# Kernel optimization log

Measured on AMD Instinct MI355X. Metric: run time of the kernel, lower is better.

## Reference

```python
import jax, jax.numpy as jnp
import numpy as np

B, N, D, K, DSPACE, NFREQ = 4, 4096, 256, 16, 3, 5
BN_EPS = 1e-5


def setup_inputs() -> dict:
    key = jax.random.key(0)
    ks = jax.random.split(key, 12)
    s = 1.0 / np.sqrt(D)
    pe_in = DSPACE * 2 * NFREQ + DSPACE  # 33
    return {
        "xyz": jax.random.normal(ks[0], (B, N, DSPACE), jnp.float32),
        "feats": jax.random.normal(ks[1], (B, N, D), jnp.float32),
        "w_q": jax.random.uniform(ks[2], (D, D), jnp.float32, -s, s),
        "w_k": jax.random.uniform(ks[3], (D, D), jnp.float32, -s, s),
        "w_v": jax.random.uniform(ks[4], (D, D), jnp.float32, -s, s),
        "g_w1": jax.random.uniform(ks[5], (D, D), jnp.float32, -s, s),
        "g_b1": jax.random.uniform(ks[6], (D,), jnp.float32, -s, s),
        "g_w2": jax.random.uniform(ks[7], (D, D), jnp.float32, -s, s),
        "g_b2": jax.random.uniform(ks[8], (D,), jnp.float32, -s, s),
        "pe_w": jax.random.uniform(ks[9], (D, pe_in), jnp.float32, -s, s),
        "pe_b": jax.random.uniform(ks[10], (D,), jnp.float32, -s, s),
        "bn_w": jnp.ones((D,), jnp.float32),
        "bn_b": jnp.zeros((D,), jnp.float32),
    }


def _gather_knn(points, idx):
    # points [b,n,c], idx [b,n,k] -> [b,n,k,c]
    return jax.vmap(lambda p, i: p[i])(points, idx)


def reference(xyz, feats, w_q, w_k, w_v, g_w1, g_b1, g_w2, g_b2, pe_w, pe_b, bn_w, bn_b):
    # KNN (no grad in original): full pairwise sq-distance + top-k smallest
    dists = jnp.sum((xyz[:, :, None] - xyz[:, None]) ** 2, axis=-1)  # [b,n,n]
    _, knn_idx = jax.lax.top_k(-dists, K)  # [b,n,k], ascending distance
    knn_idx = jax.lax.stop_gradient(knn_idx)
    knn_xyz = jax.lax.stop_gradient(_gather_knn(xyz, knn_idx))  # [b,n,k,3]

    q = feats @ w_q.T                               # [b,n,d]
    k_g = _gather_knn(feats @ w_k.T, knn_idx)       # [b,n,k,d]
    v_g = _gather_knn(feats @ w_v.T, knn_idx)       # [b,n,k,d]

    pos_diff = xyz[:, :, None] - knn_xyz            # [b,n,k,3]
    freqs = jnp.linspace(1.0, 2.0 ** NFREQ, NFREQ).astype(pos_diff.dtype)
    embeds = [pos_diff]
    for f in freqs:
        embeds.append(jnp.sin(pos_diff * f))
        embeds.append(jnp.cos(pos_diff * f))
    pos_embed = jnp.concatenate(embeds, axis=-1)    # [b,n,k,33]
    pos_encode = pos_embed @ pe_w.T + pe_b          # [b,n,k,d]

    edges = q[:, :, None] - k_g + pos_encode        # [b,n,k,d]
    h = jax.nn.relu(edges @ g_w1.T + g_b1)
    attn = h @ g_w2.T + g_b2                        # [b,n,k,d]
    attn = jax.nn.softmax(attn, axis=-2)            # softmax over neighbors

    res = jnp.einsum('bnkf,bnkf->bnf', attn, v_g + pos_encode) + feats

    # BatchNorm1d over channel dim, training-mode batch stats (biased var)
    mean = jnp.mean(res, axis=(0, 1))
    var = jnp.var(res, axis=(0, 1))
    res = (res - mean) * jax.lax.rsqrt(var + BN_EPS) * bn_w + bn_b
    return res
```

## Files before the change

kernel.cpp:

```cpp
#include <hip/hip_runtime.h>

#define BB 4
#define NN 4096
#define DD 256
#define KK 16
#define PTS 2
#define SA 280
#define SE 104

typedef __bf16 bf16;
typedef __attribute__((ext_vector_type(8))) __bf16 bf16x8;
typedef __attribute__((ext_vector_type(4))) __bf16 bf16x4;
typedef __attribute__((ext_vector_type(4))) float f32x4;

__global__ __launch_bounds__(256, 2) void setup_kernel(
    const float* __restrict__ xyz, const float* __restrict__ feats,
    const float* __restrict__ w_q, const float* __restrict__ w_k,
    const float* __restrict__ w_v, const float* __restrict__ g_w1,
    const float* __restrict__ g_w2, const float* __restrict__ pe_w,
    int* __restrict__ knn, bf16* __restrict__ qb, bf16* __restrict__ kfb,
    bf16* __restrict__ vfb, bf16* __restrict__ w1b, bf16* __restrict__ w2b,
    bf16* __restrict__ pwb, float* __restrict__ sums) {
  const int bid = blockIdx.x;
  const int t = threadIdx.x;
  __shared__ __align__(16) bf16 fs[16][SA];

  if (bid < 256) {
    const int idx = bid * 256 + t;
    w1b[idx] = (bf16)g_w1[idx];
    w2b[idx] = (bf16)g_w2[idx];
    if (idx < 256 * 64) {
      const int n = idx >> 6, c = idx & 63;
      pwb[idx] = (c < 33) ? (bf16)pe_w[n * 33 + c] : (bf16)0.f;
    }
    if (idx < 2 * DD) sums[idx] = 0.f;
    return;
  }
  if (bid < 256 + 4096) {
    const int lane = t & 63;
    const int row = (bid - 256) * 4 + (t >> 6);
    const int b = row >> 12, i = row & (NN - 1);
    const float* xb = xyz + (size_t)b * NN * 3;
    const float xi = xb[i * 3 + 0], yi = xb[i * 3 + 1], zi = xb[i * 3 + 2];
    unsigned long long cand[64];
#pragma unroll
    for (int c = 0; c < 64; ++c) {
      const int j = c * 64 + lane;
      const float dx = xi - xb[j * 3 + 0];
      const float dy = yi - xb[j * 3 + 1];
      const float dz = zi - xb[j * 3 + 2];
      const float d = dx * dx + dy * dy + dz * dz;
      const unsigned long long fb =
          (unsigned long long)(__float_as_uint(d)) + 1ull;
      cand[c] = (fb << 32) | (unsigned int)j;
    }
    unsigned long long gm[8];
#pragma unroll
    for (int g = 0; g < 8; ++g) {
      unsigned long long mn = cand[g * 8];
#pragma unroll
      for (int s = 1; s < 8; ++s)
        if (cand[g * 8 + s] < mn) mn = cand[g * 8 + s];
      gm[g] = mn;
    }
    unsigned int myj = 0u;
    for (int r = 0; r < KK; ++r) {
      unsigned long long lmin = gm[0];
#pragma unroll
      for (int g = 1; g < 8; ++g)
        if (gm[g] < lmin) lmin = gm[g];
#pragma unroll
      for (int off = 1; off < 64; off <<= 1) {
        const unsigned long long o = __shfl_xor(lmin, off);
        if (o < lmin) lmin = o;
      }
      if (lane == r) myj = (unsigned int)lmin;
#pragma unroll
      for (int g = 0; g < 8; ++g) {
        if (__ballot(gm[g] == lmin)) {
          unsigned long long nm = ~0ull;
#pragma unroll
          for (int s = 0; s < 8; ++s) {
            const unsigned long long v = cand[g * 8 + s];
            if (v > lmin && v < nm) nm = v;
          }
          if (gm[g] == lmin) gm[g] = nm;
        }
      }
    }
    if (lane < KK) knn[row * KK + lane] = (int)myj;
    return;
  }
  {
    const int lane = t & 63, wv = t >> 6;
    const int m = lane & 15, qd = lane >> 4;
    const size_t r0 = (size_t)(bid - (256 + 4096)) * 16;
    const float4* f4 = (const float4*)(feats + r0 * DD);
#pragma unroll
    for (int i = 0; i < 4; ++i) {
      const int e = i * 256 + t;
      const float4 v = f4[e];
      bf16x4 w;
      w[0] = (bf16)v.x; w[1] = (bf16)v.y; w[2] = (bf16)v.z; w[3] = (bf16)v.w;
      *(bf16x4*)&fs[e >> 6][(e & 63) * 4] = w;
    }
    __syncthreads();
    bf16x8 afrag[8];
#pragma unroll
    for (int f = 0; f < 8; ++f)
      afrag[f] = *(const bf16x8*)&fs[m][f * 32 + qd * 8];
    const float* wmat[3] = {w_q, w_k, w_v};
    bf16* omat[3] = {qb, kfb, vfb};
    for (int mat = 0; mat < 3; ++mat) {
      const float* wb = wmat[mat];
      for (int nt = 0; nt < 4; ++nt) {
        const int n = wv * 64 + nt * 16 + m;
        bf16x8 bfr[8];
#pragma unroll
        for (int f = 0; f < 8; ++f) {
          const float4 wa = *(const float4*)(wb + (size_t)n * DD + f * 32 + qd * 8);
          const float4 wc = *(const float4*)(wb + (size_t)n * DD + f * 32 + qd * 8 + 4);
          bf16x8 x;
          x[0] = (bf16)wa.x; x[1] = (bf16)wa.y; x[2] = (bf16)wa.z; x[3] = (bf16)wa.w;
          x[4] = (bf16)wc.x; x[5] = (bf16)wc.y; x[6] = (bf16)wc.z; x[7] = (bf16)wc.w;
          bfr[f] = x;
        }
        f32x4 c = {0.f, 0.f, 0.f, 0.f};
#pragma unroll
        for (int f = 0; f < 8; ++f)
          c = __builtin_amdgcn_mfma_f32_16x16x32_bf16(afrag[f], bfr[f], c, 0, 0, 0);
#pragma unroll
        for (int rr = 0; rr < 4; ++rr)
          omat[mat][(r0 + qd * 4 + rr) * DD + n] = (bf16)c[rr];
      }
    }
  }
}

__global__ __launch_bounds__(256, 3) void edge_v7(
    const float* __restrict__ xyz, const float* __restrict__ feats,
    const bf16* __restrict__ qb, const bf16* __restrict__ kfb,
    const bf16* __restrict__ vfb, const int* __restrict__ knn,
    const bf16* __restrict__ w1b, const float* __restrict__ g_b1,
    const bf16* __restrict__ w2b, const float* __restrict__ g_b2,
    const bf16* __restrict__ pwb, const float* __restrict__ pe_b,
    float* __restrict__ res, float* __restrict__ sums,
    float* __restrict__ sumsq) {
  const int t = threadIdx.x;
  const int lane = t & 63;
  const int wv = t >> 6;
  const int m = lane & 15;
  const int qd = lane >> 4;
  const int row0 = blockIdx.x * PTS;
  const int b = row0 >> 12;

  __shared__ __align__(16) bf16 bufA[PTS][16][SA];
  __shared__ __align__(16) char un_s[PTS * 16 * SA * 2];
  bf16(*bufB)[16][SA] = (bf16(*)[16][SA])un_s;
  bf16(*emb_s)[16][SE] = (bf16(*)[16][SE])un_s;
  __shared__ int js_s[PTS][16];

  if (t < PTS * 16) js_s[t >> 4][t & 15] = knn[(row0 + (t >> 4)) * KK + (t & 15)];
  __syncthreads();

  const float* xb = xyz + (size_t)b * NN * 3;
  {
    const int k = t >> 4;
    const int c0 = (t & 15) * 6;
#pragma unroll
    for (int p = 0; p < PTS; ++p) {
      const int i = (row0 + p) & (NN - 1);
      const int j = js_s[p][k];
#pragma unroll
      for (int cc = 0; cc < 6; ++cc) {
        const int c = c0 + cc;
        float val = 0.f;
        if (c < 33) {
          const int ax = (c < 3) ? c : (c - 3) % 3;
          const float pd = xb[i * 3 + ax] - xb[j * 3 + ax];
          if (c < 3) {
            val = pd;
          } else {
            const int f = (c - 3) / 6;
            const float x = pd * fmaf(7.75f, (float)f, 1.0f);
            val = (((c - 3) % 6) < 3) ? __sinf(x) : __cosf(x);
          }
        }
        emb_s[p][k][c] = (bf16)val;
      }
    }
  }
  __syncthreads();

  float vpe[4][PTS][4];
  bf16x8 ea0[PTS], ea1[PTS];
#pragma unroll
  for (int p = 0; p < PTS; ++p) {
    ea0[p] = *(const bf16x8*)&emb_s[p][m][qd * 8];
    ea1[p] = *(const bf16x8*)&emb_s[p][m][32 + qd * 8];
  }
#pragma unroll
  for (int tt = 0; tt < 4; ++tt) {
    const int n = wv * 64 + tt * 16 + m;
    const bf16x8 b0 = *(const bf16x8*)(pwb + (size_t)n * 64 + qd * 8);
    const bf16x8 b1 = *(const bf16x8*)(pwb + (size_t)n * 64 + 32 + qd * 8);
    const float bias = pe_b[n];
#pragma unroll
    for (int p = 0; p < PTS; ++p) {
      f32x4 c = {bias, bias, bias, bias};
      c = __builtin_amdgcn_mfma_f32_16x16x32_bf16(ea0[p], b0, c, 0, 0, 0);
      c = __builtin_amdgcn_mfma_f32_16x16x32_bf16(ea1[p], b1, c, 0, 0, 0);
      const float qv = (float)qb[(size_t)(row0 + p) * DD + n];
#pragma unroll
      for (int rr = 0; rr < 4; ++rr) {
        const int krow = qd * 4 + rr;
        const size_t jr = ((size_t)(b * NN + js_s[p][krow])) * DD + n;
        bufA[p][krow][n] = (bf16)(qv - (float)kfb[jr] + c[rr]);
        vpe[tt][p][rr] = (float)vfb[jr] + c[rr];
      }
    }
  }
  __syncthreads();

  {
    bf16x8 afrag[PTS][8];
#pragma unroll
    for (int p = 0; p < PTS; ++p)
#pragma unroll
      for (int f = 0; f < 8; ++f)
        afrag[p][f] = *(const bf16x8*)&bufA[p][m][f * 32 + qd * 8];
    for (int tt = 0; tt < 4; ++tt) {
      const int n = wv * 64 + tt * 16 + m;
      bf16x8 bfr[8];
#pragma unroll
      for (int f = 0; f < 8; ++f)
        bfr[f] = *(const bf16x8*)(w1b + (size_t)n * DD + f * 32 + qd * 8);
      const float bias = g_b1[n];
#pragma unroll
      for (int p = 0; p < PTS; ++p) {
        f32x4 c = {bias, bias, bias, bias};
#pragma unroll
        for (int f = 0; f < 8; ++f)
          c = __builtin_amdgcn_mfma_f32_16x16x32_bf16(afrag[p][f], bfr[f], c, 0, 0, 0);
#pragma unroll
        for (int rr = 0; rr < 4; ++rr)
          bufB[p][qd * 4 + rr][n] = (bf16)fmaxf(c[rr], 0.f);
      }
    }
  }
  __syncthreads();

  {
    bf16x8 afrag[PTS][8];
#pragma unroll
    for (int p = 0; p < PTS; ++p)
#pragma unroll
      for (int f = 0; f < 8; ++f)
        afrag[p][f] = *(const bf16x8*)&bufB[p][m][f * 32 + qd * 8];
#pragma unroll
    for (int tt = 0; tt < 4; ++tt) {
      const int n = wv * 64 + tt * 16 + m;
      bf16x8 bfr[8];
#pragma unroll
      for (int f = 0; f < 8; ++f)
        bfr[f] = *(const bf16x8*)(w2b + (size_t)n * DD + f * 32 + qd * 8);
      const float bias = g_b2[n];
      float bs = 0.f, bs2 = 0.f;
#pragma unroll
      for (int p = 0; p < PTS; ++p) {
        f32x4 c = {bias, bias, bias, bias};
#pragma unroll
        for (int f = 0; f < 8; ++f)
          c = __builtin_amdgcn_mfma_f32_16x16x32_bf16(afrag[p][f], bfr[f], c, 0, 0, 0);
        float mx = fmaxf(fmaxf(c[0], c[1]), fmaxf(c[2], c[3]));
        mx = fmaxf(mx, __shfl_xor(mx, 16));
        mx = fmaxf(mx, __shfl_xor(mx, 32));
        float e[4], den = 0.f;
#pragma unroll
        for (int rr = 0; rr < 4; ++rr) {
          e[rr] = __expf(c[rr] - mx);
          den += e[rr];
        }
        den += __shfl_xor(den, 16);
        den += __shfl_xor(den, 32);
        float num = 0.f;
#pragma unroll
        for (int rr = 0; rr < 4; ++rr) num += e[rr] * vpe[tt][p][rr];
        num += __shfl_xor(num, 16);
        num += __shfl_xor(num, 32);
        if (qd == 0) {
          const size_t o = (size_t)(row0 + p) * DD + n;
          const float out = num / den + feats[o];
          res[o] = out;
          bs += out;
          bs2 += out * out;
        }
      }
      if (qd == 0) {
        atomicAdd(&sums[n], bs);
        atomicAdd(&sumsq[n], bs2);
      }
    }
  }
}

__global__ __launch_bounds__(256) void bn_apply(float* __restrict__ out,
                                                const float* __restrict__ sums,
                                                const float* __restrict__ sumsq,
                                                const float* __restrict__ bn_w,
                                                const float* __restrict__ bn_b) {
  const int idx = blockIdx.x * 256 + threadIdx.x;
  const int c = idx & (DD - 1);
  const float inv_n = 1.f / (float)(BB * NN);
  const float mean = sums[c] * inv_n;
  const float var = sumsq[c] * inv_n - mean * mean;
  const float v = out[idx];
  out[idx] = (v - mean) * rsqrtf(var + 1e-5f) * bn_w[c] + bn_b[c];
}

extern "C" void kernel_launch(void* const* d_in, const int* in_sizes, int n_in,
                              void* d_out, int out_size, void* d_ws,
                              size_t ws_size, hipStream_t stream) {
  (void)in_sizes; (void)n_in; (void)out_size; (void)ws_size;
  const float* xyz = (const float*)d_in[0];
  const float* feats = (const float*)d_in[1];
  const float* w_q = (const float*)d_in[2];
  const float* w_k = (const float*)d_in[3];
  const float* w_v = (const float*)d_in[4];
  const float* g_w1 = (const float*)d_in[5];
  const float* g_b1 = (const float*)d_in[6];
  const float* g_w2 = (const float*)d_in[7];
  const float* g_b2 = (const float*)d_in[8];
  const float* pe_w = (const float*)d_in[9];
  const float* pe_b = (const float*)d_in[10];
  const float* bn_w = (const float*)d_in[11];
  const float* bn_b = (const float*)d_in[12];
  float* out = (float*)d_out;

  const int BN = BB * NN;
  char* w = (char*)d_ws;
  int* knn = (int*)w;       w += (size_t)BN * KK * 4;
  bf16* qb = (bf16*)w;      w += (size_t)BN * DD * 2;
  bf16* kfb = (bf16*)w;     w += (size_t)BN * DD * 2;
  bf16* vfb = (bf16*)w;     w += (size_t)BN * DD * 2;
  float* sums = (float*)w;  w += DD * 4;
  float* sumsq = (float*)w; w += DD * 4;
  bf16* w1b = (bf16*)w;     w += (size_t)DD * DD * 2;
  bf16* w2b = (bf16*)w;     w += (size_t)DD * DD * 2;
  bf16* pwb = (bf16*)w;     w += (size_t)DD * 64 * 2;

  setup_kernel<<<256 + 4096 + 1024, 256, 0, stream>>>(
      xyz, feats, w_q, w_k, w_v, g_w1, g_w2, pe_w, knn, qb, kfb, vfb, w1b, w2b,
      pwb, sums);
  edge_v7<<<BN / PTS, 256, 0, stream>>>(xyz, feats, qb, kfb, vfb, knn, w1b,
                                        g_b1, w2b, g_b2, pwb, pe_b, out, sums,
                                        sumsq);
  bn_apply<<<BN, 256, 0, stream>>>(out, sums, sumsq, bn_w, bn_b);
}
```

Baseline: 648.5 us.

## Stage xyz in LDS for KNN, enlarge projection tiles, use 512-thread edge blocks

In the setup kernel, the KNN branch now copies the whole batch's xyz into shared memory before the distance loop, replacing strided global reads. The projection branch handles 64 rows per block instead of 16, so each converted weight fragment is reused across four waves, and the block roles are reordered. The edge kernel moves to 512 threads per block, with each wave covering 32 output columns instead of 64, to cut per-thread register use and raise parallelism. The costs are a 48KB shared-memory staging copy per KNN block (limiting occupancy) and heavier LDS pressure per block in the edge kernel.

After: 907.2 us. 1.4x slower.

```diff
diff --git a/kernel.cpp b/kernel.cpp
--- a/kernel.cpp
+++ b/kernel.cpp
@@ -6,12 +6,16 @@
 #define KK 16
 #define PTS 2
 #define SA 280
-#define SE 104
+#define SE 96
 
 typedef __bf16 bf16;
 typedef __attribute__((ext_vector_type(8))) __bf16 bf16x8;
 typedef __attribute__((ext_vector_type(4))) __bf16 bf16x4;
 typedef __attribute__((ext_vector_type(4))) float f32x4;
+
+#define KNNB 4096
+#define PROJB 256
+#define PREPB 256
 
 __global__ __launch_bounds__(256, 2) void setup_kernel(
     const float* __restrict__ xyz, const float* __restrict__ feats,
@@ -23,10 +27,117 @@
     bf16* __restrict__ pwb, float* __restrict__ sums) {
   const int bid = blockIdx.x;
   const int t = threadIdx.x;
-  __shared__ __align__(16) bf16 fs[16][SA];
-
-  if (bid < 256) {
-    const int idx = bid * 256 + t;
+  __shared__ __align__(16) float smem[NN * 3];
+
+  if (bid < KNNB) {
+    const int row0 = bid * 4;
+    const int b = row0 >> 12;
+    const float* xb = xyz + (size_t)b * NN * 3;
+    for (int e = t; e < NN * 3; e += 256) smem[e] = xb[e];
+    __syncthreads();
+    const int lane = t & 63;
+    const int row = row0 + (t >> 6);
+    const int i = row & (NN - 1);
+    const float xi = smem[i * 3 + 0], yi = smem[i * 3 + 1], zi = smem[i * 3 + 2];
+    unsigned long long cand[64];
+#pragma unroll
+    for (int c = 0; c < 64; ++c) {
+      const int j = c * 64 + lane;
+      const float dx = xi - smem[j * 3 + 0];
+      const float dy = yi - smem[j * 3 + 1];
+      const float dz = zi - smem[j * 3 + 2];
+      const float d = dx * dx + dy * dy + dz * dz;
+      const unsigned long long fb =
+          (unsigned long long)(__float_as_uint(d)) + 1ull;
+      cand[c] = (fb << 32) | (unsigned int)j;
+    }
+    unsigned long long gm[8];
+#pragma unroll
+    for (int g = 0; g < 8; ++g) {
+      unsigned long long mn = cand[g * 8];
+#pragma unroll
+      for (int s = 1; s < 8; ++s)
+        if (cand[g * 8 + s] < mn) mn = cand[g * 8 + s];
+      gm[g] = mn;
+    }
+    unsigned int myj = 0u;
+    for (int r = 0; r < KK; ++r) {
+      unsigned long long lmin = gm[0];
+#pragma unroll
+      for (int g = 1; g < 8; ++g)
+        if (gm[g] < lmin) lmin = gm[g];
+#pragma unroll
+      for (int off = 1; off < 64; off <<= 1) {
+        const unsigned long long o = __shfl_xor(lmin, off);
+        if (o < lmin) lmin = o;
+      }
+      if (lane == r) myj = (unsigned int)lmin;
+#pragma unroll
+      for (int g = 0; g < 8; ++g) {
+        if (__ballot(gm[g] == lmin)) {
+          unsigned long long nm = ~0ull;
+#pragma unroll
+          for (int s = 0; s < 8; ++s) {
+            const unsigned long long v = cand[g * 8 + s];
+            if (v > lmin && v < nm) nm = v;
+          }
+          if (gm[g] == lmin) gm[g] = nm;
+        }
+      }
+    }
+    if (lane < KK) knn[row * KK + lane] = (int)myj;
+    return;
+  }
+  if (bid < KNNB + PROJB) {
+    bf16(*fs)[264] = (bf16(*)[264])smem;
+    const int lane = t & 63, wv = t >> 6;
+    const int m = lane & 15, qd = lane >> 4;
+    const size_t r0 = (size_t)(bid - KNNB) * 64;
+    const float4* f4 = (const float4*)(feats + r0 * DD);
+#pragma unroll
+    for (int i = 0; i < 16; ++i) {
+      const int e = i * 256 + t;
+      const float4 v = f4[e];
+      bf16x4 w;
+      w[0] = (bf16)v.x; w[1] = (bf16)v.y; w[2] = (bf16)v.z; w[3] = (bf16)v.w;
+      *(bf16x4*)&fs[e >> 6][(e & 63) * 4] = w;
+    }
+    __syncthreads();
+    bf16x8 afrag[8];
+#pragma unroll
+    for (int f = 0; f < 8; ++f)
+      afrag[f] = *(const bf16x8*)&fs[wv * 16 + m][f * 32 + qd * 8];
+    const float* wmat[3] = {w_q, w_k, w_v};
+    bf16* omat[3] = {qb, kfb, vfb};
+    for (int mat = 0; mat < 3; ++mat) {
+      const float* wb = wmat[mat];
+      for (int nt = 0; nt < 16; ++nt) {
+        const int n = nt * 16 + m;
+        bf16x8 bfr[8];
+#pragma unroll
+        for (int f = 0; f < 8; ++f) {
+          const float4 wa =
+              *(const float4*)(wb + (size_t)n * DD + f * 32 + qd * 8);
+          const float4 wc =
+              *(const float4*)(wb + (size_t)n * DD + f * 32 + qd * 8 + 4);
+          bf16x8 x;
+          x[0] = (bf16)wa.x; x[1] = (bf16)wa.y; x[2] = (bf16)wa.z; x[3] = (bf16)wa.w;
+          x[4] = (bf16)wc.x; x[5] = (bf16)wc.y; x[6] = (bf16)wc.z; x[7] = (bf16)wc.w;
+          bfr[f] = x;
+        }
+        f32x4 c = {0.f, 0.f, 0.f, 0.f};
+#pragma unroll
+        for (int f = 0; f < 8; ++f)
+          c = __builtin_amdgcn_mfma_f32_16x16x32_bf16(afrag[f], bfr[f], c, 0, 0, 0);
+#pragma unroll
+        for (int rr = 0; rr < 4; ++rr)
+          omat[mat][(r0 + wv * 16 + qd * 4 + rr) * DD + n] = (bf16)c[rr];
+      }
+    }
+    return;
+  }
+  {
+    const int idx = (bid - (KNNB + PROJB)) * 256 + t;
     w1b[idx] = (bf16)g_w1[idx];
     w2b[idx] = (bf16)g_w2[idx];
     if (idx < 256 * 64) {
@@ -34,110 +145,10 @@
       pwb[idx] = (c < 33) ? (bf16)pe_w[n * 33 + c] : (bf16)0.f;
     }
     if (idx < 2 * DD) sums[idx] = 0.f;
-    return;
-  }
-  if (bid < 256 + 4096) {
-    const int lane = t & 63;
-    const int row = (bid - 256) * 4 + (t >> 6);
-    const int b = row >> 12, i = row & (NN - 1);
-    const float* xb = xyz + (size_t)b * NN * 3;
-    const float xi = xb[i * 3 + 0], yi = xb[i * 3 + 1], zi = xb[i * 3 + 2];
-    unsigned long long cand[64];
-#pragma unroll
-    for (int c = 0; c < 64; ++c) {
-      const int j = c * 64 + lane;
-      const float dx = xi - xb[j * 3 + 0];
-      const float dy = yi - xb[j * 3 + 1];
-      const float dz = zi - xb[j * 3 + 2];
-      const float d = dx * dx + dy * dy + dz * dz;
-      const unsigned long long fb =
-          (unsigned long long)(__float_as_uint(d)) + 1ull;
-      cand[c] = (fb << 32) | (unsigned int)j;
-    }
-    unsigned long long gm[8];
-#pragma unroll
-    for (int g = 0; g < 8; ++g) {
-      unsigned long long mn = cand[g * 8];
-#pragma unroll
-      for (int s = 1; s < 8; ++s)
-        if (cand[g * 8 + s] < mn) mn = cand[g * 8 + s];
-      gm[g] = mn;
-    }
-    unsigned int myj = 0u;
-    for (int r = 0; r < KK; ++r) {
-      unsigned long long lmin = gm[0];
-#pragma unroll
-      for (int g = 1; g < 8; ++g)
-        if (gm[g] < lmin) lmin = gm[g];
-#pragma unroll
-      for (int off = 1; off < 64; off <<= 1) {
-        const unsigned long long o = __shfl_xor(lmin, off);
-        if (o < lmin) lmin = o;
-      }
-      if (lane == r) myj = (unsigned int)lmin;
-#pragma unroll
-      for (int g = 0; g < 8; ++g) {
-        if (__ballot(gm[g] == lmin)) {
-          unsigned long long nm = ~0ull;
-#pragma unroll
-          for (int s = 0; s < 8; ++s) {
-            const unsigned long long v = cand[g * 8 + s];
-            if (v > lmin && v < nm) nm = v;
-          }
-          if (gm[g] == lmin) gm[g] = nm;
-        }
-      }
-    }
-    if (lane < KK) knn[row * KK + lane] = (int)myj;
-    return;
-  }
-  {
-    const int lane = t & 63, wv = t >> 6;
-    const int m = lane & 15, qd = lane >> 4;
-    const size_t r0 = (size_t)(bid - (256 + 4096)) * 16;
-    const float4* f4 = (const float4*)(feats + r0 * DD);
-#pragma unroll
-    for (int i = 0; i < 4; ++i) {
-      const int e = i * 256 + t;
-      const float4 v = f4[e];
-      bf16x4 w;
-      w[0] = (bf16)v.x; w[1] = (bf16)v.y; w[2] = (bf16)v.z; w[3] = (bf16)v.w;
-      *(bf16x4*)&fs[e >> 6][(e & 63) * 4] = w;
-    }
-    __syncthreads();
-    bf16x8 afrag[8];
-#pragma unroll
-    for (int f = 0; f < 8; ++f)
-      afrag[f] = *(const bf16x8*)&fs[m][f * 32 + qd * 8];
-    const float* wmat[3] = {w_q, w_k, w_v};
-    bf16* omat[3] = {qb, kfb, vfb};
-    for (int mat = 0; mat < 3; ++mat) {
-      const float* wb = wmat[mat];
-      for (int nt = 0; nt < 4; ++nt) {
-        const int n = wv * 64 + nt * 16 + m;
-        bf16x8 bfr[8];
-#pragma unroll
-        for (int f = 0; f < 8; ++f) {
-          const float4 wa = *(const float4*)(wb + (size_t)n * DD + f * 32 + qd * 8);
-          const float4 wc = *(const float4*)(wb + (size_t)n * DD + f * 32 + qd * 8 + 4);
-          bf16x8 x;
-          x[0] = (bf16)wa.x; x[1] = (bf16)wa.y; x[2] = (bf16)wa.z; x[3] = (bf16)wa.w;
-          x[4] = (bf16)wc.x; x[5] = (bf16)wc.y; x[6] = (bf16)wc.z; x[7] = (bf16)wc.w;
-          bfr[f] = x;
-        }
-        f32x4 c = {0.f, 0.f, 0.f, 0.f};
-#pragma unroll
-        for (int f = 0; f < 8; ++f)
-          c = __builtin_amdgcn_mfma_f32_16x16x32_bf16(afrag[f], bfr[f], c, 0, 0, 0);
-#pragma unroll
-        for (int rr = 0; rr < 4; ++rr)
-          omat[mat][(r0 + qd * 4 + rr) * DD + n] = (bf16)c[rr];
-      }
-    }
   }
 }
 
-__global__ __launch_bounds__(256, 3) void edge_v7(
+__global__ __launch_bounds__(512, 6) void edge_v8(
     const float* __restrict__ xyz, const float* __restrict__ feats,
     const bf16* __restrict__ qb, const bf16* __restrict__ kfb,
     const bf16* __restrict__ vfb, const int* __restrict__ knn,
@@ -165,14 +176,14 @@
 
   const float* xb = xyz + (size_t)b * NN * 3;
   {
-    const int k = t >> 4;
-    const int c0 = (t & 15) * 6;
+    const int k = t >> 5;
+    const int c0 = (t & 31) * 3;
 #pragma unroll
     for (int p = 0; p < PTS; ++p) {
       const int i = (row0 + p) & (NN - 1);
       const int j = js_s[p][k];
 #pragma unroll
-      for (int cc = 0; cc < 6; ++cc) {
+      for (int cc = 0; cc < 3; ++cc) {
         const int c = c0 + cc;
         float val = 0.f;
         if (c < 33) {
@@ -192,7 +203,7 @@
   }
   __syncthreads();
 
-  float vpe[4][PTS][4];
+  float vpe[2][PTS][4];
   bf16x8 ea0[PTS], ea1[PTS];
 #pragma unroll
   for (int p = 0; p < PTS; ++p) {
@@ -200,8 +211,8 @@
     ea1[p] = *(const bf16x8*)&emb_s[p][m][32 + qd * 8];
   }
 #pragma unroll
-  for (int tt = 0; tt < 4; ++tt) {
-    const int n = wv * 64 + tt * 16 + m;
+  for (int tt = 0; tt < 2; ++tt) {
+    const int n = wv * 32 + tt * 16 + m;
     const bf16x8 b0 = *(const bf16x8*)(pwb + (size_t)n * 64 + qd * 8);
     const bf16x8 b1 = *(const bf16x8*)(pwb + (size_t)n * 64 + 32 + qd * 8);
     const float bias = pe_b[n];
@@ -229,8 +240,8 @@
 #pragma unroll
       for (int f = 0; f < 8; ++f)
         afrag[p][f] = *(const bf16x8*)&bufA[p][m][f * 32 + qd * 8];
-    for (int tt = 0; tt < 4; ++tt) {
-      const int n = wv * 64 + tt * 16 + m;
+    for (int tt = 0; tt < 2; ++tt) {
+      const int n = wv * 32 + tt * 16 + m;
       bf16x8 bfr[8];
 #pragma unroll
       for (int f = 0; f < 8; ++f)
@@ -258,8 +269,8 @@
       for (int f = 0; f < 8; ++f)
         afrag[p][f] = *(const bf16x8*)&bufB[p][m][f * 32 + qd * 8];
 #pragma unroll
-    for (int tt = 0; tt < 4; ++tt) {
-      const int n = wv * 64 + tt * 16 + m;
+    for (int tt = 0; tt < 2; ++tt) {
+      const int n = wv * 32 + tt * 16 + m;
       bf16x8 bfr[8];
 #pragma unroll
       for (int f = 0; f < 8; ++f)
@@ -349,10 +360,10 @@
   bf16* w2b = (bf16*)w;     w += (size_t)DD * DD * 2;
   bf16* pwb = (bf16*)w;     w += (size_t)DD * 64 * 2;
 
-  setup_kernel<<<256 + 4096 + 1024, 256, 0, stream>>>(
+  setup_kernel<<<KNNB + PROJB + PREPB, 256, 0, stream>>>(
       xyz, feats, w_q, w_k, w_v, g_w1, g_w2, pe_w, knn, qb, kfb, vfb, w1b, w2b,
       pwb, sums);
-  edge_v7<<<BN / PTS, 256, 0, stream>>>(xyz, feats, qb, kfb, vfb, knn, w1b,
+  edge_v8<<<BN / PTS, 512, 0, stream>>>(xyz, feats, qb, kfb, vfb, knn, w1b,
                                         g_b1, w2b, g_b2, pwb, pe_b, out, sums,
                                         sumsq);
   bn_apply<<<BN, 256, 0, stream>>>(out, sums, sumsq, bn_w, bn_b);
```
